# Kernel tuning notes

Hardware: AMD Instinct MI355X
Metric: run time of the kernel (lower is better)

Reference implementation:

```python
import jax, jax.numpy as jnp
import numpy as np

B, T, DIN, DOUT = 32, 3136, 192, 384
H, QS, WS = 6, 4, 16            # heads, q_stride, window_size (post-pool)
HD = DOUT // H                   # head_dim = 64
INNER = QS * WS                  # tokens per mask unit before pooling = 64
NW = T // INNER                  # num_windows = 49
MLP_HID = 4 * DOUT
EPS = 1e-5


def layer_norm(x, w, b):
    mu = x.mean(-1, keepdims=True)
    var = ((x - mu) ** 2).mean(-1, keepdims=True)
    return (x - mu) * jax.lax.rsqrt(var + EPS) * w + b


def setup_inputs() -> dict:
    key = jax.random.key(0)
    ks = jax.random.split(key, 16)
    rn = lambda k, shp, fan: jax.random.normal(k, shp, jnp.float32) * (fan ** -0.5)
    return {
        "embeddings": jax.random.normal(ks[0], (B, T, DIN), jnp.float32),
        "norm1_w": jnp.ones((DIN,), jnp.float32),
        "norm1_b": jnp.zeros((DIN,), jnp.float32),
        "w_qkv": rn(ks[1], (3 * DOUT, DIN), DIN),
        "b_qkv": jnp.zeros((3 * DOUT,), jnp.float32),
        "w_attn_proj": rn(ks[2], (DOUT, DOUT), DOUT),
        "b_attn_proj": jnp.zeros((DOUT,), jnp.float32),
        "w_res_proj": rn(ks[3], (DOUT, DIN), DIN),
        "b_res_proj": jnp.zeros((DOUT,), jnp.float32),
        "norm2_w": jnp.ones((DOUT,), jnp.float32),
        "norm2_b": jnp.zeros((DOUT,), jnp.float32),
        "w_fc1": rn(ks[4], (MLP_HID, DOUT), DOUT),
        "b_fc1": jnp.zeros((MLP_HID,), jnp.float32),
        "w_fc2": rn(ks[5], (DOUT, MLP_HID), MLP_HID),
        "b_fc2": jnp.zeros((DOUT,), jnp.float32),
    }


def _block(embeddings, norm1_w, norm1_b, w_qkv, b_qkv, w_attn_proj, b_attn_proj,
           w_res_proj, b_res_proj, norm2_w, norm2_b, w_fc1, b_fc1, w_fc2, b_fc2):
    x = layer_norm(embeddings, norm1_w, norm1_b)                 # [B,T,DIN]

    # residual path: project then do_pool (max over q_stride groups)
    res = x @ w_res_proj.T + b_res_proj                          # [B,T,DOUT]
    res = res.reshape(B, QS, T // QS, DOUT).max(axis=1)          # [B,T/QS,DOUT]

    # mask-unit attention
    qkv = x @ w_qkv.T + b_qkv                                    # [B,T,3*DOUT]
    qkv = qkv.reshape(B, INNER, NW, 3, H, HD)
    qkv = jnp.transpose(qkv, (3, 0, 4, 2, 1, 5))                 # [3,B,H,NW,INNER,HD]
    q, k, v = qkv[0], qkv[1], qkv[2]
    q = q.reshape(B, H, NW, QS, WS, HD).max(axis=3)              # q-pool -> [B,H,NW,WS,HD]
    scale = HD ** -0.5
    attn = jax.nn.softmax(jnp.einsum("bhwqd,bhwkd->bhwqk", q * scale, k), axis=-1)
    out = jnp.einsum("bhwqk,bhwkd->bhwqd", attn, v)              # [B,H,NW,WS,HD]
    out = jnp.transpose(out, (0, 3, 2, 1, 4)).reshape(B, WS * NW, DOUT)
    out = out @ w_attn_proj.T + b_attn_proj

    emb = res + out
    h = layer_norm(emb, norm2_w, norm2_b)
    h = jax.nn.gelu(h @ w_fc1.T + b_fc1, approximate=False)
    emb = emb + (h @ w_fc2.T + b_fc2)
    return emb, attn


def reference(embeddings, norm1_w, norm1_b, w_qkv, b_qkv, w_attn_proj, b_attn_proj,
              w_res_proj, b_res_proj, norm2_w, norm2_b, w_fc1, b_fc1, w_fc2, b_fc2):
    return _block(embeddings, norm1_w, norm1_b, w_qkv, b_qkv, w_attn_proj, b_attn_proj,
                  w_res_proj, b_res_proj, norm2_w, norm2_b, w_fc1, b_fc1, w_fc2, b_fc2)
```

## Files before the change

### kernel.cpp

```cpp
#include <hip/hip_runtime.h>
#include <stdint.h>

typedef __bf16 bf16_t;
typedef __attribute__((ext_vector_type(8))) __bf16 bf16x8;
typedef __attribute__((ext_vector_type(4))) __bf16 bf16x4;
typedef __attribute__((ext_vector_type(4))) float f32x4;

#define NB_ 32
#define NT_ 3136
#define DIN_ 192
#define DOUT_ 384
#define NH_ 6
#define HD_ 64
#define NW_ 49
#define WSZ_ 16
#define TP_ 784
#define MLP_ 1536

__device__ __forceinline__ f32x4 mfma16(bf16x8 a, bf16x8 b, f32x4 c) {
  return __builtin_amdgcn_mfma_f32_16x16x32_bf16(a, b, c, 0, 0, 0);
}

__device__ __forceinline__ void gload_lds16(const bf16_t* g, bf16_t* l) {
  __builtin_amdgcn_global_load_lds(
      (const __attribute__((address_space(1))) void*)((const void*)g),
      (__attribute__((address_space(3))) void*)l, 16, 0, 0);
}

__global__ void cvt_kernel(const float* __restrict__ s0, const float* __restrict__ s1,
                           const float* __restrict__ s2, const float* __restrict__ s3,
                           const float* __restrict__ s4, bf16_t* __restrict__ d0,
                           bf16_t* __restrict__ d1, bf16_t* __restrict__ d2,
                           bf16_t* __restrict__ d3, bf16_t* __restrict__ d4) {
  const int b = blockIdx.x;
  const float* s; bf16_t* d; long off;
  if (b < 108)      { s = s0; d = d0; off = (long)b * 2048; }
  else if (b < 144) { s = s1; d = d1; off = (long)(b - 108) * 2048; }
  else if (b < 216) { s = s2; d = d2; off = (long)(b - 144) * 2048; }
  else if (b < 504) { s = s3; d = d3; off = (long)(b - 216) * 2048; }
  else              { s = s4; d = d4; off = (long)(b - 504) * 2048; }
  off += (long)threadIdx.x * 8;
  const float4 a = *(const float4*)(s + off);
  const float4 c = *(const float4*)(s + off + 4);
  bf16x8 o;
  o[0] = (bf16_t)a.x; o[1] = (bf16_t)a.y; o[2] = (bf16_t)a.z; o[3] = (bf16_t)a.w;
  o[4] = (bf16_t)c.x; o[5] = (bf16_t)c.y; o[6] = (bf16_t)c.z; o[7] = (bf16_t)c.w;
  *(bf16x8*)(d + off) = o;
}

template <int D>
__global__ void ln_f32_kernel(const float* __restrict__ in, const float* __restrict__ w,
                              const float* __restrict__ bvec, bf16_t* __restrict__ out) {
  const int row = blockIdx.x * 4 + (threadIdx.x >> 6);
  const int lane = threadIdx.x & 63;
  constexpr int PER = D / 64;
  const float* x = in + (long)row * D;
  float v[PER];
  float s = 0.f;
#pragma unroll
  for (int i = 0; i < PER; i++) { v[i] = x[lane * PER + i]; s += v[i]; }
#pragma unroll
  for (int off = 1; off < 64; off <<= 1) s += __shfl_xor(s, off);
  const float mu = s * (1.f / D);
  float s2 = 0.f;
#pragma unroll
  for (int i = 0; i < PER; i++) { const float d = v[i] - mu; s2 += d * d; }
#pragma unroll
  for (int off = 1; off < 64; off <<= 1) s2 += __shfl_xor(s2, off);
  const float rstd = rsqrtf(s2 * (1.f / D) + 1e-5f);
  bf16_t* o = out + (long)row * D;
#pragma unroll
  for (int i = 0; i < PER; i++) {
    const int c = lane * PER + i;
    o[c] = (bf16_t)((v[i] - mu) * rstd * w[c] + bvec[c]);
  }
}

template <int D>
__global__ void ln_bf16_kernel(const bf16_t* __restrict__ in, const float* __restrict__ w,
                               const float* __restrict__ bvec, bf16_t* __restrict__ out) {
  const int row = blockIdx.x * 4 + (threadIdx.x >> 6);
  const int lane = threadIdx.x & 63;
  constexpr int PER = D / 64;
  const bf16_t* x = in + (long)row * D;
  float v[PER];
  float s = 0.f;
#pragma unroll
  for (int i = 0; i < PER; i++) { v[i] = (float)x[lane * PER + i]; s += v[i]; }
#pragma unroll
  for (int off = 1; off < 64; off <<= 1) s += __shfl_xor(s, off);
  const float mu = s * (1.f / D);
  float s2 = 0.f;
#pragma unroll
  for (int i = 0; i < PER; i++) { const float d = v[i] - mu; s2 += d * d; }
#pragma unroll
  for (int off = 1; off < 64; off <<= 1) s2 += __shfl_xor(s2, off);
  const float rstd = rsqrtf(s2 * (1.f / D) + 1e-5f);
  bf16_t* o = out + (long)row * D;
#pragma unroll
  for (int i = 0; i < PER; i++) {
    const int c = lane * PER + i;
    o[c] = (bf16_t)((v[i] - mu) * rstd * w[c] + bvec[c]);
  }
}

template <int ACT, int HASRES, int POOL, int OF32, int RF32>
__global__ __launch_bounds__(512, 4) void gemm8(
    const bf16_t* __restrict__ A, const bf16_t* __restrict__ W,
    const float* __restrict__ bias, const void* __restrict__ resv,
    void* __restrict__ Cv, int M, int N, int K) {
  __shared__ __align__(16) char AsB[256 * 128];
  __shared__ __align__(16) char WsB[128 * 128];

  const int nwg = gridDim.x;
  const int q = nwg >> 3, rm = nwg & 7;
  const int xcd = blockIdx.x & 7, idx = blockIdx.x >> 3;
  const int wg = (xcd < rm ? xcd * (q + 1) : rm * (q + 1) + (xcd - rm) * q) + idx;

  const int nbn = N >> 7;
  const int bmi = wg / nbn;
  const int bni = wg - bmi * nbn;
  const int m0 = bmi << 8, n0 = bni << 7;
  const int tid = threadIdx.x;
  const int lane = tid & 63;
  const int wid = tid >> 6;
  const int wr = (wid >> 1) * 64, wc = (wid & 1) * 64;
  const int l15 = lane & 15;
  const int lkb = (lane >> 4) << 4;
  const int srow = tid >> 3;
  const int scolsw = ((tid & 7) << 3) ^ ((srow & 7) << 3);
  const int swzr = (l15 & 7) << 4;

  f32x4 acc[4][4];
  const f32x4 zero = {0.f, 0.f, 0.f, 0.f};
#pragma unroll
  for (int i = 0; i < 4; i++)
#pragma unroll
    for (int j = 0; j < 4; j++) acc[i][j] = zero;

  long arow[4];
#pragma unroll
  for (int p = 0; p < 4; p++) {
    const int m = m0 + p * 64 + srow;
    if constexpr (POOL) {
      const int b = m / NT_;
      const int mm = m - b * NT_;
      arow[p] = (long)b * NT_ + (mm & 3) * TP_ + (mm >> 2);
    } else {
      arow[p] = m;
    }
  }
  long wrow[2];
#pragma unroll
  for (int p = 0; p < 2; p++) wrow[p] = (long)(n0 + p * 64 + srow);

  for (int k0 = 0; k0 < K; k0 += 64) {
    __syncthreads();
#pragma unroll
    for (int p = 0; p < 4; p++)
      gload_lds16(A + arow[p] * K + k0 + scolsw, (bf16_t*)(AsB + p * 8192 + tid * 16));
#pragma unroll
    for (int p = 0; p < 2; p++)
      gload_lds16(W + wrow[p] * K + k0 + scolsw, (bf16_t*)(WsB + p * 8192 + tid * 16));
    __syncthreads();
#pragma unroll
    for (int kk = 0; kk < 2; kk++) {
      bf16x8 af[4], wf[4];
#pragma unroll
      for (int i = 0; i < 4; i++)
        af[i] = *(const bf16x8*)(AsB + (wr + i * 16 + l15) * 128 + ((kk * 64 + lkb) ^ swzr));
#pragma unroll
      for (int j = 0; j < 4; j++)
        wf[j] = *(const bf16x8*)(WsB + (wc + j * 16 + l15) * 128 + ((kk * 64 + lkb) ^ swzr));
#pragma unroll
      for (int i = 0; i < 4; i++)
#pragma unroll
        for (int j = 0; j < 4; j++) {
          if constexpr (POOL) acc[i][j] = mfma16(af[i], wf[j], acc[i][j]);
          else                acc[i][j] = mfma16(wf[j], af[i], acc[i][j]);
        }
    }
  }

  const int rg = (lane >> 4) * 4;
  if constexpr (POOL) {
#pragma unroll
    for (int j = 0; j < 4; j++) {
      const int gn = n0 + wc + j * 16 + l15;
      const float bv = bias[gn];
#pragma unroll
      for (int i = 0; i < 4; i++) {
        const float v = fmaxf(fmaxf(acc[i][j][0], acc[i][j][1]),
                              fmaxf(acc[i][j][2], acc[i][j][3])) + bv;
        const long pm = (long)((m0 + wr + i * 16 + rg) >> 2);
        ((bf16_t*)Cv)[pm * N + gn] = (bf16_t)v;
      }
    }
  } else {
#pragma unroll
    for (int i = 0; i < 4; i++) {
      const long gm = m0 + wr + i * 16 + l15;
#pragma unroll
      for (int j = 0; j < 4; j++) {
        const int gn = n0 + wc + j * 16 + rg;
        const float4 bv = *(const float4*)(bias + gn);
        float v[4] = {acc[i][j][0] + bv.x, acc[i][j][1] + bv.y,
                      acc[i][j][2] + bv.z, acc[i][j][3] + bv.w};
        if constexpr (ACT == 1) {
#pragma unroll
          for (int r = 0; r < 4; r++) {
            const float t2 = 1.5957691216f * (v[r] + 0.044715f * v[r] * v[r] * v[r]);
            v[r] = v[r] * (1.f - 1.f / (1.f + __expf(t2)));
          }
        }
        if constexpr (HASRES) {
          if constexpr (RF32) {
            const float4 rv = *(const float4*)((const float*)resv + gm * N + gn);
            v[0] += rv.x; v[1] += rv.y; v[2] += rv.z; v[3] += rv.w;
          } else {
            const bf16x4 rv = *(const bf16x4*)((const bf16_t*)resv + gm * N + gn);
#pragma unroll
            for (int r = 0; r < 4; r++) v[r] += (float)rv[r];
          }
        }
        if constexpr (OF32) {
          float4 o = {v[0], v[1], v[2], v[3]};
          *(float4*)((float*)Cv + gm * N + gn) = o;
        } else {
          bf16x4 o;
#pragma unroll
          for (int r = 0; r < 4; r++) o[r] = (bf16_t)v[r];
          *(bf16x4*)((bf16_t*)Cv + gm * N + gn) = o;
        }
      }
    }
  }
}

template <int ACT, int HASRES, int POOL, int OF32, int RF32, int BM>
__global__ __launch_bounds__(256) void gemm_t(
    const bf16_t* __restrict__ A, const bf16_t* __restrict__ W,
    const float* __restrict__ bias, const void* __restrict__ resv,
    void* __restrict__ Cv, int M, int N, int K) {
  constexpr int PA = BM / 32;
  constexpr int ABYTES = BM * 128;
  constexpr int BUFSZ = ABYTES + 128 * 128;
  __shared__ __align__(16) char LDSB[2 * BUFSZ];

  const int nwg = gridDim.x;
  const int q = nwg >> 3, rm = nwg & 7;
  const int xcd = blockIdx.x & 7, idx = blockIdx.x >> 3;
  const int wg = (xcd < rm ? xcd * (q + 1) : rm * (q + 1) + (xcd - rm) * q) + idx;

  const int nbn = N >> 7;
  const int bmi = wg / nbn;
  const int bni = wg - bmi * nbn;
  const int m0 = bmi * BM, n0 = bni << 7;
  const int tid = threadIdx.x;
  const int lane = tid & 63;
  const int wid = tid >> 6;
  const int wr = (wid >> 1) * (BM / 2), wc = (wid & 1) * 64;
  const int l15 = lane & 15;
  const int lkb = (lane >> 4) << 4;
  const int srow = tid >> 3;
  const int scolsw = ((tid & 7) << 3) ^ ((srow & 7) << 3);
  const int swzr = (l15 & 7) << 4;

  f32x4 acc[PA][4];
  const f32x4 zero = {0.f, 0.f, 0.f, 0.f};
#pragma unroll
  for (int i = 0; i < PA; i++)
#pragma unroll
    for (int j = 0; j < 4; j++) acc[i][j] = zero;

  long arow[PA];
#pragma unroll
  for (int p = 0; p < PA; p++) {
    const int m = m0 + srow + p * 32;
    if constexpr (POOL) {
      const int b = m / NT_;
      const int mm = m - b * NT_;
      arow[p] = (long)b * NT_ + (mm & 3) * TP_ + (mm >> 2);
    } else {
      arow[p] = m;
    }
  }
  long wrow[4];
#pragma unroll
  for (int p = 0; p < 4; p++) wrow[p] = (long)(n0 + srow + p * 32);

  auto stage = [&](int buf, int k0) {
    char* base = LDSB + buf * BUFSZ;
#pragma unroll
    for (int p = 0; p < PA; p++)
      gload_lds16(A + arow[p] * K + k0 + scolsw, (bf16_t*)(base + p * 4096 + tid * 16));
#pragma unroll
    for (int p = 0; p < 4; p++)
      gload_lds16(W + wrow[p] * K + k0 + scolsw,
                  (bf16_t*)(base + ABYTES + p * 4096 + tid * 16));
  };

  const int nt = K >> 6;
  stage(0, 0);
  int cur = 0;
  for (int t = 0; t < nt; t++) {
    __syncthreads();
    if (t + 1 < nt) stage(cur ^ 1, (t + 1) << 6);
    const char* base = LDSB + cur * BUFSZ;
#pragma unroll
    for (int kk = 0; kk < 2; kk++) {
      bf16x8 af[PA], wf[4];
#pragma unroll
      for (int i = 0; i < PA; i++)
        af[i] = *(const bf16x8*)(base + (wr + i * 16 + l15) * 128 + ((kk * 64 + lkb) ^ swzr));
#pragma unroll
      for (int j = 0; j < 4; j++)
        wf[j] = *(const bf16x8*)(base + ABYTES + (wc + j * 16 + l15) * 128 +
                                 ((kk * 64 + lkb) ^ swzr));
#pragma unroll
      for (int i = 0; i < PA; i++)
#pragma unroll
        for (int j = 0; j < 4; j++) {
          if constexpr (POOL) acc[i][j] = mfma16(af[i], wf[j], acc[i][j]);
          else                acc[i][j] = mfma16(wf[j], af[i], acc[i][j]);
        }
    }
    cur ^= 1;
  }

  const int rg = (lane >> 4) * 4;
  if constexpr (POOL) {
#pragma unroll
    for (int j = 0; j < 4; j++) {
      const int gn = n0 + wc + j * 16 + l15;
      const float bv = bias[gn];
#pragma unroll
      for (int i = 0; i < PA; i++) {
        const float v = fmaxf(fmaxf(acc[i][j][0], acc[i][j][1]),
                              fmaxf(acc[i][j][2], acc[i][j][3])) + bv;
        const long pm = (long)((m0 + wr + i * 16 + rg) >> 2);
        ((bf16_t*)Cv)[pm * N + gn] = (bf16_t)v;
      }
    }
  } else {
#pragma unroll
    for (int i = 0; i < PA; i++) {
      const long gm = m0 + wr + i * 16 + l15;
#pragma unroll
      for (int j = 0; j < 4; j++) {
        const int gn = n0 + wc + j * 16 + rg;
        const float4 bv = *(const float4*)(bias + gn);
        float v[4] = {acc[i][j][0] + bv.x, acc[i][j][1] + bv.y,
                      acc[i][j][2] + bv.z, acc[i][j][3] + bv.w};
        if constexpr (ACT == 1) {
#pragma unroll
          for (int r = 0; r < 4; r++) {
            const float t2 = 1.5957691216f * (v[r] + 0.044715f * v[r] * v[r] * v[r]);
            v[r] = v[r] * (1.f - 1.f / (1.f + __expf(t2)));
          }
        }
        if constexpr (HASRES) {
          if constexpr (RF32) {
            const float4 rv = *(const float4*)((const float*)resv + gm * N + gn);
            v[0] += rv.x; v[1] += rv.y; v[2] += rv.z; v[3] += rv.w;
          } else {
            const bf16x4 rv = *(const bf16x4*)((const bf16_t*)resv + gm * N + gn);
#pragma unroll
            for (int r = 0; r < 4; r++) v[r] += (float)rv[r];
          }
        }
        if constexpr (OF32) {
          float4 o = {v[0], v[1], v[2], v[3]};
          *(float4*)((float*)Cv + gm * N + gn) = o;
        } else {
          bf16x4 o;
#pragma unroll
          for (int r = 0; r < 4; r++) o[r] = (bf16_t)v[r];
          *(bf16x4*)((bf16_t*)Cv + gm * N + gn) = o;
        }
      }
    }
  }
}

__global__ __launch_bounds__(256) void attn_kernel(const bf16_t* __restrict__ qkv,
                                                   float* __restrict__ attn_out,
                                                   bf16_t* __restrict__ obuf) {
  __shared__ __align__(16) bf16_t Vs[4][64 * 64];
  __shared__ __align__(16) bf16_t Ps[4][16 * 64];
  const int wid = threadIdx.x >> 6;
  const int lane = threadIdx.x & 63;
  const int flat = blockIdx.x * 4 + wid;
  const int w = flat % NW_;
  const int h = (flat / NW_) % NH_;
  const int b = flat / (NW_ * NH_);
  const int l15 = lane & 15, lk8 = (lane >> 4) * 8;
  const bf16_t* qb = qkv + (long)b * NT_ * (3 * DOUT_);
  bf16_t* Vw = Vs[wid];
  bf16_t* Pw = Ps[wid];

#pragma unroll
  for (int p = 0; p < 8; p++) {
    const int inner = p * 8 + (lane >> 3);
    const int col = (lane & 7) * 8;
    const bf16x8 t =
        *(const bf16x8*)(qb + (long)(inner * NW_ + w) * (3 * DOUT_) + 2 * DOUT_ + h * HD_ + col);
    *(bf16x8*)&Vw[p * 512 + lane * 8] = t;
  }

  bf16x8 aq[2];
#pragma unroll
  for (int kc = 0; kc < 2; kc++) {
    const int d = kc * 32 + lk8;
    float qv[8];
#pragma unroll
    for (int e = 0; e < 8; e++) qv[e] = -1e30f;
#pragma unroll
    for (int qs = 0; qs < 4; qs++) {
      const bf16x8 t =
          *(const bf16x8*)(qb + (long)((qs * 16 + l15) * NW_ + w) * (3 * DOUT_) + h * HD_ + d);
#pragma unroll
      for (int e = 0; e < 8; e++) qv[e] = fmaxf(qv[e], (float)t[e]);
    }
    bf16x8 a;
#pragma unroll
    for (int e = 0; e < 8; e++) a[e] = (bf16_t)(qv[e] * 0.125f);
    aq[kc] = a;
  }

  f32x4 s4[4];
  const f32x4 zero = {0.f, 0.f, 0.f, 0.f};
#pragma unroll
  for (int nc = 0; nc < 4; nc++) s4[nc] = zero;
#pragma unroll
  for (int nc = 0; nc < 4; nc++) {
#pragma unroll
    for (int kc = 0; kc < 2; kc++) {
      const int tok = nc * 16 + l15;
      const int d = kc * 32 + lk8;
      const bf16x8 bk =
          *(const bf16x8*)(qb + (long)(tok * NW_ + w) * (3 * DOUT_) + DOUT_ + h * HD_ + d);
      s4[nc] = mfma16(aq[kc], bk, s4[nc]);
    }
  }

#pragma unroll
  for (int r = 0; r < 4; r++) {
    float mx = fmaxf(fmaxf(s4[0][r], s4[1][r]), fmaxf(s4[2][r], s4[3][r]));
#pragma unroll
    for (int off = 1; off < 16; off <<= 1) mx = fmaxf(mx, __shfl_xor(mx, off));
    float sm = 0.f;
#pragma unroll
    for (int nc = 0; nc < 4; nc++) {
      const float p = __expf(s4[nc][r] - mx);
      s4[nc][r] = p;
      sm += p;
    }
#pragma unroll
    for (int off = 1; off < 16; off <<= 1) sm += __shfl_xor(sm, off);
    const float inv = 1.f / sm;
#pragma unroll
    for (int nc = 0; nc < 4; nc++) s4[nc][r] *= inv;
  }

  const int rg = (lane >> 4) * 4;
  float* aout = attn_out + (long)flat * (WSZ_ * 64);
#pragma unroll
  for (int nc = 0; nc < 4; nc++) {
#pragma unroll
    for (int r = 0; r < 4; r++) {
      const int row = rg + r, col = nc * 16 + l15;
      aout[row * 64 + col] = s4[nc][r];
      Pw[row * 64 + col] = (bf16_t)s4[nc][r];
    }
  }

  bf16x8 ap[2];
#pragma unroll
  for (int kc = 0; kc < 2; kc++) ap[kc] = *(const bf16x8*)&Pw[l15 * 64 + kc * 32 + lk8];

  f32x4 o4[4];
#pragma unroll
  for (int nc = 0; nc < 4; nc++) o4[nc] = zero;
#pragma unroll
  for (int nc = 0; nc < 4; nc++) {
#pragma unroll
    for (int kc = 0; kc < 2; kc++) {
      bf16x8 bv;
#pragma unroll
      for (int e = 0; e < 8; e++) bv[e] = Vw[(kc * 32 + lk8 + e) * 64 + nc * 16 + l15];
      o4[nc] = mfma16(ap[kc], bv, o4[nc]);
    }
  }

  bf16_t* ob = obuf + (long)b * TP_ * DOUT_;
#pragma unroll
  for (int nc = 0; nc < 4; nc++) {
#pragma unroll
    for (int r = 0; r < 4; r++) {
      const int wsr = rg + r;
      const int tprime = wsr * NW_ + w;
      const int chan = h * HD_ + nc * 16 + l15;
      ob[(long)tprime * DOUT_ + chan] = (bf16_t)o4[nc][r];
    }
  }
}

extern "C" void kernel_launch(void* const* d_in, const int* in_sizes, int n_in,
                              void* d_out, int out_size, void* d_ws, size_t ws_size,
                              hipStream_t stream) {
  const float* emb   = (const float*)d_in[0];
  const float* n1w   = (const float*)d_in[1];
  const float* n1b   = (const float*)d_in[2];
  const float* wqkv  = (const float*)d_in[3];
  const float* bqkv  = (const float*)d_in[4];
  const float* wproj = (const float*)d_in[5];
  const float* bproj = (const float*)d_in[6];
  const float* wres  = (const float*)d_in[7];
  const float* bres  = (const float*)d_in[8];
  const float* n2w   = (const float*)d_in[9];
  const float* n2b   = (const float*)d_in[10];
  const float* wfc1  = (const float*)d_in[11];
  const float* bfc1  = (const float*)d_in[12];
  const float* wfc2  = (const float*)d_in[13];
  const float* bfc2  = (const float*)d_in[14];
  float* out = (float*)d_out;

  const int BT = NB_ * NT_;
  const int BTP = NB_ * TP_;
  const int BSL = 8;
  const int MSL = BSL * NT_;

  char* wsb = (char*)d_ws;
  bf16_t* qkvb = (bf16_t*)(wsb);
  bf16_t* h1   = (bf16_t*)(wsb);
  bf16_t* obuf = (bf16_t*)(wsb + 57802752L);
  bf16_t* resp = (bf16_t*)(wsb + 77070336L);
  bf16_t* h0   = resp;
  bf16_t* emb1 = (bf16_t*)(wsb + 96337920L);
  bf16_t* wbqkv = (bf16_t*)(wsb + 115605504L);
  bf16_t* wbres = wbqkv + 221184L;
  bf16_t* wbproj = wbres + 73728L;
  bf16_t* wbfc1 = wbproj + 147456L;
  bf16_t* wbfc2 = wbfc1 + 589824L;
  float*  prob = out + 9633792L;
  bf16_t* x    = (bf16_t*)(out + 9633792L);

  cvt_kernel<<<792, 256, 0, stream>>>(wqkv, wres, wproj, wfc1, wfc2,
                                      wbqkv, wbres, wbproj, wbfc1, wbfc2);
  ln_f32_kernel<DIN_><<<BT / 4, 256, 0, stream>>>(emb, n1w, n1b, x);
  gemm8<0, 0, 1, 0, 0><<<(BT / 256) * (DOUT_ / 128), 512, 0, stream>>>(
      x, wbres, bres, nullptr, resp, BT, DOUT_, DIN_);
  for (int s = 0; s < 4; s++) {
    gemm8<0, 0, 0, 0, 0><<<(MSL / 256) * (3 * DOUT_ / 128), 512, 0, stream>>>(
        x + (long)s * MSL * DIN_, wbqkv, bqkv, nullptr, qkvb, MSL, 3 * DOUT_, DIN_);
    attn_kernel<<<BSL * NH_ * NW_ / 4, 256, 0, stream>>>(
        qkvb, prob + (long)s * 2408448L, obuf + (long)s * 2408448L);
  }
  gemm_t<0, 1, 0, 0, 0, 64><<<(BTP / 64) * (DOUT_ / 128), 256, 0, stream>>>(
      obuf, wbproj, bproj, resp, emb1, BTP, DOUT_, DOUT_);
  ln_bf16_kernel<DOUT_><<<BTP / 4, 256, 0, stream>>>(emb1, n2w, n2b, h0);
  gemm8<1, 0, 0, 0, 0><<<(BTP / 256) * (MLP_ / 128), 512, 0, stream>>>(
      h0, wbfc1, bfc1, nullptr, h1, BTP, MLP_, DOUT_);
  gemm_t<0, 1, 0, 1, 0, 64><<<(BTP / 64) * (DOUT_ / 128), 256, 0, stream>>>(
      h1, wbfc2, bfc2, emb1, out, BTP, DOUT_, MLP_);
}
```

Measured before the change: 384.9 us.

## Fuse LayerNorm2, FC1+GELU and FC2+residual into a single MLP kernel

Replaces the separate LayerNorm, FC1 GEMM with GELU, and FC2 GEMM launches with one kernel that handles 64 rows per block. The block normalizes rows into swizzled LDS, computes 192-wide hidden chunks with GELU into LDS, and accumulates FC2 in registers, so the hidden activation and the normalized input never travel through global memory. In exchange, weights are read straight from global memory into registers with no LDS staging, every block re-reads all of W1 and W2, and each block holds large accumulators, which can reduce occupancy and MFMA efficiency.

```diff
diff --git a/kernel.cpp b/kernel.cpp
--- a/kernel.cpp
+++ b/kernel.cpp
@@ -76,34 +76,6 @@
   }
 }
 
-template <int D>
-__global__ void ln_bf16_kernel(const bf16_t* __restrict__ in, const float* __restrict__ w,
-                               const float* __restrict__ bvec, bf16_t* __restrict__ out) {
-  const int row = blockIdx.x * 4 + (threadIdx.x >> 6);
-  const int lane = threadIdx.x & 63;
-  constexpr int PER = D / 64;
-  const bf16_t* x = in + (long)row * D;
-  float v[PER];
-  float s = 0.f;
-#pragma unroll
-  for (int i = 0; i < PER; i++) { v[i] = (float)x[lane * PER + i]; s += v[i]; }
-#pragma unroll
-  for (int off = 1; off < 64; off <<= 1) s += __shfl_xor(s, off);
-  const float mu = s * (1.f / D);
-  float s2 = 0.f;
-#pragma unroll
-  for (int i = 0; i < PER; i++) { const float d = v[i] - mu; s2 += d * d; }
-#pragma unroll
-  for (int off = 1; off < 64; off <<= 1) s2 += __shfl_xor(s2, off);
-  const float rstd = rsqrtf(s2 * (1.f / D) + 1e-5f);
-  bf16_t* o = out + (long)row * D;
-#pragma unroll
-  for (int i = 0; i < PER; i++) {
-    const int c = lane * PER + i;
-    o[c] = (bf16_t)((v[i] - mu) * rstd * w[c] + bvec[c]);
-  }
-}
-
 template <int ACT, int HASRES, int POOL, int OF32, int RF32>
 __global__ __launch_bounds__(512, 4) void gemm8(
     const bf16_t* __restrict__ A, const bf16_t* __restrict__ W,
@@ -206,13 +178,6 @@
         const float4 bv = *(const float4*)(bias + gn);
         float v[4] = {acc[i][j][0] + bv.x, acc[i][j][1] + bv.y,
                       acc[i][j][2] + bv.z, acc[i][j][3] + bv.w};
-        if constexpr (ACT == 1) {
-#pragma unroll
-          for (int r = 0; r < 4; r++) {
-            const float t2 = 1.5957691216f * (v[r] + 0.044715f * v[r] * v[r] * v[r]);
-            v[r] = v[r] * (1.f - 1.f / (1.f + __expf(t2)));
-          }
-        }
         if constexpr (HASRES) {
           if constexpr (RF32) {
             const float4 rv = *(const float4*)((const float*)resv + gm * N + gn);
@@ -352,13 +317,6 @@
         const float4 bv = *(const float4*)(bias + gn);
         float v[4] = {acc[i][j][0] + bv.x, acc[i][j][1] + bv.y,
                       acc[i][j][2] + bv.z, acc[i][j][3] + bv.w};
-        if constexpr (ACT == 1) {
-#pragma unroll
-          for (int r = 0; r < 4; r++) {
-            const float t2 = 1.5957691216f * (v[r] + 0.044715f * v[r] * v[r] * v[r]);
-            v[r] = v[r] * (1.f - 1.f / (1.f + __expf(t2)));
-          }
-        }
         if constexpr (HASRES) {
           if constexpr (RF32) {
             const float4 rv = *(const float4*)((const float*)resv + gm * N + gn);
@@ -379,6 +337,140 @@
           *(bf16x4*)((bf16_t*)Cv + gm * N + gn) = o;
         }
       }
+    }
+  }
+}
+
+__global__ __launch_bounds__(256) void mlp_kernel(
+    const bf16_t* __restrict__ emb1, const float* __restrict__ n2w,
+    const float* __restrict__ n2b, const bf16_t* __restrict__ W1,
+    const float* __restrict__ b1, const bf16_t* __restrict__ W2,
+    const float* __restrict__ b2, float* __restrict__ outp) {
+  __shared__ __align__(16) char As[64 * 768];
+  __shared__ __align__(16) char Hs[64 * 384];
+  const int m0 = blockIdx.x * 64;
+  const int tid = threadIdx.x;
+  const int lane = tid & 63;
+  const int wid = tid >> 6;
+  const int l15 = lane & 15;
+  const int lk8 = (lane >> 4) * 8;
+  const int lkb = (lane >> 4) << 4;
+  const int rg = (lane >> 4) * 4;
+  const f32x4 zero = {0.f, 0.f, 0.f, 0.f};
+
+  {
+    const int row = tid >> 2, qq = tid & 3;
+    const bf16_t* src = emb1 + (long)(m0 + row) * DOUT_ + qq * 96;
+    bf16x8 vv[12];
+    float s = 0.f;
+#pragma unroll
+    for (int i = 0; i < 12; i++) {
+      vv[i] = *(const bf16x8*)(src + i * 8);
+#pragma unroll
+      for (int e = 0; e < 8; e++) s += (float)vv[i][e];
+    }
+    s += __shfl_xor(s, 1); s += __shfl_xor(s, 2);
+    const float mu = s * (1.f / DOUT_);
+    float s2 = 0.f;
+#pragma unroll
+    for (int i = 0; i < 12; i++)
+#pragma unroll
+      for (int e = 0; e < 8; e++) { const float d = (float)vv[i][e] - mu; s2 += d * d; }
+    s2 += __shfl_xor(s2, 1); s2 += __shfl_xor(s2, 2);
+    const float rstd = rsqrtf(s2 * (1.f / DOUT_) + 1e-5f);
+    const int swz = (row & 7) << 4;
+#pragma unroll
+    for (int i = 0; i < 12; i++) {
+      const int col = qq * 96 + i * 8;
+      const float4 w0 = *(const float4*)(n2w + col);
+      const float4 w1 = *(const float4*)(n2w + col + 4);
+      const float4 c0 = *(const float4*)(n2b + col);
+      const float4 c1 = *(const float4*)(n2b + col + 4);
+      const float wv[8] = {w0.x, w0.y, w0.z, w0.w, w1.x, w1.y, w1.z, w1.w};
+      const float bv[8] = {c0.x, c0.y, c0.z, c0.w, c1.x, c1.y, c1.z, c1.w};
+      bf16x8 o;
+#pragma unroll
+      for (int e = 0; e < 8; e++)
+        o[e] = (bf16_t)(((float)vv[i][e] - mu) * rstd * wv[e] + bv[e]);
+      *(bf16x8*)(As + row * 768 + ((col * 2) ^ swz)) = o;
+    }
+  }
+
+  f32x4 acc[4][6];
+#pragma unroll
+  for (int i = 0; i < 4; i++)
+#pragma unroll
+    for (int j = 0; j < 6; j++) acc[i][j] = zero;
+
+  for (int c = 0; c < 8; c++) {
+    __syncthreads();
+#pragma unroll
+    for (int nj = 0; nj < 3; nj++) {
+      const int hn = c * 192 + wid * 48 + nj * 16 + l15;
+      const int nloc = wid * 48 + nj * 16 + l15;
+      bf16x8 wfr[12];
+#pragma unroll
+      for (int ks = 0; ks < 12; ks++)
+        wfr[ks] = *(const bf16x8*)(W1 + (long)hn * DOUT_ + ks * 32 + lk8);
+      f32x4 a1[4];
+#pragma unroll
+      for (int i = 0; i < 4; i++) a1[i] = zero;
+#pragma unroll
+      for (int ks = 0; ks < 12; ks++) {
+#pragma unroll
+        for (int i = 0; i < 4; i++) {
+          const int mr = i * 16 + l15;
+          const bf16x8 af = *(const bf16x8*)(As + mr * 768 +
+                                             ((ks * 64 + lkb) ^ ((mr & 7) << 4)));
+          a1[i] = mfma16(af, wfr[ks], a1[i]);
+        }
+      }
+      const float bb = b1[hn];
+      const int blk = (2 * nloc) >> 4, win = (2 * nloc) & 15;
+#pragma unroll
+      for (int i = 0; i < 4; i++) {
+#pragma unroll
+        for (int r = 0; r < 4; r++) {
+          float v = a1[i][r] + bb;
+          const float t2 = 1.5957691216f * (v + 0.044715f * v * v * v);
+          v = v * (1.f - 1.f / (1.f + __expf(t2)));
+          const int m = i * 16 + rg + r;
+          *(bf16_t*)(Hs + m * 384 + ((blk ^ (m & 7)) << 4) + win) = (bf16_t)v;
+        }
+      }
+    }
+    __syncthreads();
+#pragma unroll
+    for (int j = 0; j < 6; j++) {
+      const int on = wid * 96 + j * 16 + l15;
+      bf16x8 wfr2[6];
+#pragma unroll
+      for (int ks = 0; ks < 6; ks++)
+        wfr2[ks] = *(const bf16x8*)(W2 + (long)on * MLP_ + c * 192 + ks * 32 + lk8);
+#pragma unroll
+      for (int ks = 0; ks < 6; ks++) {
+#pragma unroll
+        for (int i = 0; i < 4; i++) {
+          const int mr = i * 16 + l15;
+          const bf16x8 af = *(const bf16x8*)(Hs + mr * 384 +
+                                             ((ks * 64 + lkb) ^ ((mr & 7) << 4)));
+          acc[i][j] = mfma16(wfr2[ks], af, acc[i][j]);
+        }
+      }
+    }
+  }
+
+#pragma unroll
+  for (int i = 0; i < 4; i++) {
+    const long gm = m0 + i * 16 + l15;
+#pragma unroll
+    for (int j = 0; j < 6; j++) {
+      const int gn = wid * 96 + j * 16 + rg;
+      const float4 bv = *(const float4*)(b2 + gn);
+      const bf16x4 rv = *(const bf16x4*)(emb1 + gm * DOUT_ + gn);
+      float4 o = {acc[i][j][0] + bv.x + (float)rv[0], acc[i][j][1] + bv.y + (float)rv[1],
+                  acc[i][j][2] + bv.z + (float)rv[2], acc[i][j][3] + bv.w + (float)rv[3]};
+      *(float4*)(outp + gm * DOUT_ + gn) = o;
     }
   }
 }
@@ -533,10 +625,8 @@
 
   char* wsb = (char*)d_ws;
   bf16_t* qkvb = (bf16_t*)(wsb);
-  bf16_t* h1   = (bf16_t*)(wsb);
   bf16_t* obuf = (bf16_t*)(wsb + 57802752L);
   bf16_t* resp = (bf16_t*)(wsb + 77070336L);
-  bf16_t* h0   = resp;
   bf16_t* emb1 = (bf16_t*)(wsb + 96337920L);
   bf16_t* wbqkv = (bf16_t*)(wsb + 115605504L);
   bf16_t* wbres = wbqkv + 221184L;
@@ -559,9 +649,6 @@
   }
   gemm_t<0, 1, 0, 0, 0, 64><<<(BTP / 64) * (DOUT_ / 128), 256, 0, stream>>>(
       obuf, wbproj, bproj, resp, emb1, BTP, DOUT_, DOUT_);
-  ln_bf16_kernel<DOUT_><<<BTP / 4, 256, 0, stream>>>(emb1, n2w, n2b, h0);
-  gemm8<1, 0, 0, 0, 0><<<(BTP / 256) * (MLP_ / 128), 512, 0, stream>>>(
-      h0, wbfc1, bfc1, nullptr, h1, BTP, MLP_, DOUT_);
-  gemm_t<0, 1, 0, 1, 0, 64><<<(BTP / 64) * (DOUT_ / 128), 256, 0, stream>>>(
-      h1, wbfc2, bfc2, emb1, out, BTP, DOUT_, MLP_);
-}
+  mlp_kernel<<<BTP / 64, 256, 0, stream>>>(emb1, n2w, n2b, wbfc1, bfc1,
+                                           wbfc2, bfc2, out);
+}
```

After: 519.2 us. 34.9% more time.
